# Performance work log

Hardware: AMD Instinct MI355X
Metric: run time of the kernel (lower is better)

## Reference

```python
import jax, jax.numpy as jnp
import numpy as np

# pywt db2 decomposition filters (mode='symmetric', pywt defaults)
DEC_LO = np.array([-0.12940952255092145, 0.22414386804185735,
                   0.836516303737469, 0.48296291314469025], dtype=np.float32)
DEC_HI = np.array([-0.48296291314469025, 0.836516303737469,
                   -0.22414386804185735, -0.12940952255092145], dtype=np.float32)


def _dwt_axis(x, filt, axis):
    """Single-level 1D DWT along `axis`, symmetric padding, matching pywt.

    Equivalent to: symmetric-pad by F-1 each side, full convolution with
    `filt` (true convolution => filter flipped), take indices 1,3,5,...
    Implemented as pad (F-2, F-1) + strided correlation with reversed filter.
    """
    F = filt.shape[0]
    x = jnp.moveaxis(x, axis, -1)
    N = x.shape[-1]
    out_len = (N + F - 1) // 2
    pad = [(0, 0)] * (x.ndim - 1) + [(F - 2, F - 1)]
    xp = jnp.pad(x, pad, mode='symmetric')
    filt_rev = filt[::-1]
    # sum of 4 strided slices (F=4) -- fully vectorized, no big intermediates
    out = filt_rev[0] * xp[..., 0:2 * out_len:2]
    for k in range(1, F):
        out = out + filt_rev[k] * xp[..., k:k + 2 * out_len:2]
    return jnp.moveaxis(out, -1, axis)


def setup_inputs() -> dict:
    key = jax.random.key(0)
    x = jax.random.normal(key, (16, 3, 1024, 1024), dtype=jnp.float32)
    return {"x": x}


def reference(x):
    lo = jnp.asarray(DEC_LO)
    hi = jnp.asarray(DEC_HI)
    # pywt.dwt2 -> cA = 'aa' (approx rows, approx cols),
    #              cH = 'da' (detail along axis -2, approx along axis -1)
    lo_rows = _dwt_axis(x, lo, -2)
    hi_rows = _dwt_axis(x, hi, -2)
    cA = _dwt_axis(lo_rows, lo, -1)
    cH = _dwt_axis(hi_rows, lo, -1)
    return (cA, cH)
```

## Files before the change

### kernel.cpp

```cpp
#include <hip/hip_runtime.h>


#define N 1024
#define NOUT 513
#define TI 8
#define STRIPS ((NOUT + TI - 1) / TI)

__device__ __forceinline__ int refl(int p) {
    int r = p - 2;
    r = (r < 0) ? (-1 - r) : r;
    r = (r > N - 1) ? (2 * N - 1 - r) : r;
    return r;
}

__device__ __forceinline__ float4 comb4(float w0, const float4 a, float w1, const float4 b,
                                        float w2, const float4 c, float w3, const float4 d) {
    float4 r;
    r.x = fmaf(w0, a.x, fmaf(w1, b.x, fmaf(w2, c.x, w3 * d.x)));
    r.y = fmaf(w0, a.y, fmaf(w1, b.y, fmaf(w2, c.y, w3 * d.y)));
    r.z = fmaf(w0, a.z, fmaf(w1, b.z, fmaf(w2, c.z, w3 * d.z)));
    r.w = fmaf(w0, a.w, fmaf(w1, b.w, fmaf(w2, c.w, w3 * d.w)));
    return r;
}

__device__ __forceinline__ float2 comb2(float w0, const float2 a, float w1, const float2 b,
                                        float w2, const float2 c, float w3, const float2 d) {
    float2 r;
    r.x = fmaf(w0, a.x, fmaf(w1, b.x, fmaf(w2, c.x, w3 * d.x)));
    r.y = fmaf(w0, a.y, fmaf(w1, b.y, fmaf(w2, c.y, w3 * d.y)));
    return r;
}

__global__ __launch_bounds__(128, 4) void dwt2_nolds(const float* __restrict__ x,
                                                     float* __restrict__ out) {
    const float l0 =  0.48296291314469025f;
    const float l1 =  0.836516303737469f;
    const float l2 =  0.22414386804185735f;
    const float l3 = -0.12940952255092145f;
    const float h0 = -0.12940952255092145f;
    const float h1 = -0.22414386804185735f;
    const float h2 =  0.836516303737469f;
    const float h3 = -0.48296291314469025f;

    const int strip = blockIdx.x;
    const int img   = blockIdx.y;
    const int i0 = strip * TI;
    const int u  = threadIdx.x;
    const int c  = 8 * u;
    const int ce = (u == 0) ? 0 : (c - 2);

    const float* xim = x + (size_t)img * N * N;
    const size_t plane = (size_t)NOUT * NOUT;
    float* cA = out + (size_t)img * plane;
    float* cH = out + ((size_t)48 + img) * plane;

    const int nrows = (NOUT - i0 < TI) ? (NOUT - i0) : TI;

    const float* p0 = xim + (size_t)refl(2 * i0)     * N;
    const float* p1 = xim + (size_t)refl(2 * i0 + 1) * N;
    const float* p2 = xim + (size_t)refl(2 * i0 + 2) * N;
    const float* p3 = xim + (size_t)refl(2 * i0 + 3) * N;

    float4 r0a = *reinterpret_cast<const float4*>(p0 + c);
    float4 r0b = *reinterpret_cast<const float4*>(p0 + c + 4);
    float2 r0e = *reinterpret_cast<const float2*>(p0 + ce);
    float4 r1a = *reinterpret_cast<const float4*>(p1 + c);
    float4 r1b = *reinterpret_cast<const float4*>(p1 + c + 4);
    float2 r1e = *reinterpret_cast<const float2*>(p1 + ce);
    float4 n0a = *reinterpret_cast<const float4*>(p2 + c);
    float4 n0b = *reinterpret_cast<const float4*>(p2 + c + 4);
    float2 n0e = *reinterpret_cast<const float2*>(p2 + ce);
    float4 n1a = *reinterpret_cast<const float4*>(p3 + c);
    float4 n1b = *reinterpret_cast<const float4*>(p3 + c + 4);
    float2 n1e = *reinterpret_cast<const float2*>(p3 + ce);

    for (int ii = 0; ii < nrows; ++ii) {
        const int i = i0 + ii;

        float4 vloA = comb4(l0, r0a, l1, r1a, l2, n0a, l3, n1a);
        float4 vloB = comb4(l0, r0b, l1, r1b, l2, n0b, l3, n1b);
        float2 plo  = comb2(l0, r0e, l1, r1e, l2, n0e, l3, n1e);
        float4 vhiA = comb4(h0, r0a, h1, r1a, h2, n0a, h3, n1a);
        float4 vhiB = comb4(h0, r0b, h1, r1b, h2, n0b, h3, n1b);
        float2 phi  = comb2(h0, r0e, h1, r1e, h2, n0e, h3, n1e);

        if (u == 0) {
            plo = make_float2(vloA.y, vloA.x);
            phi = make_float2(vhiA.y, vhiA.x);
        }

        r0a = n0a; r0b = n0b; r0e = n0e;
        r1a = n1a; r1b = n1b; r1e = n1e;
        if (ii + 1 < nrows) {
            const float* q0 = xim + (size_t)refl(2 * i + 4) * N;
            const float* q1 = xim + (size_t)refl(2 * i + 5) * N;
            n0a = *reinterpret_cast<const float4*>(q0 + c);
            n0b = *reinterpret_cast<const float4*>(q0 + c + 4);
            n0e = *reinterpret_cast<const float2*>(q0 + ce);
            n1a = *reinterpret_cast<const float4*>(q1 + c);
            n1b = *reinterpret_cast<const float4*>(q1 + c + 4);
            n1e = *reinterpret_cast<const float2*>(q1 + ce);
        }

        float oA0 = fmaf(l0, plo.x,  fmaf(l1, plo.y,  fmaf(l2, vloA.x, l3 * vloA.y)));
        float oA1 = fmaf(l0, vloA.x, fmaf(l1, vloA.y, fmaf(l2, vloA.z, l3 * vloA.w)));
        float oA2 = fmaf(l0, vloA.z, fmaf(l1, vloA.w, fmaf(l2, vloB.x, l3 * vloB.y)));
        float oA3 = fmaf(l0, vloB.x, fmaf(l1, vloB.y, fmaf(l2, vloB.z, l3 * vloB.w)));
        float oH0 = fmaf(l0, phi.x,  fmaf(l1, phi.y,  fmaf(l2, vhiA.x, l3 * vhiA.y)));
        float oH1 = fmaf(l0, vhiA.x, fmaf(l1, vhiA.y, fmaf(l2, vhiA.z, l3 * vhiA.w)));
        float oH2 = fmaf(l0, vhiA.z, fmaf(l1, vhiA.w, fmaf(l2, vhiB.x, l3 * vhiB.y)));
        float oH3 = fmaf(l0, vhiB.x, fmaf(l1, vhiB.y, fmaf(l2, vhiB.z, l3 * vhiB.w)));

        float* pa = cA + (size_t)i * NOUT + 4 * u;
        float* ph = cH + (size_t)i * NOUT + 4 * u;
        pa[0] = oA0; pa[1] = oA1; pa[2] = oA2; pa[3] = oA3;
        ph[0] = oH0; ph[1] = oH1; ph[2] = oH2; ph[3] = oH3;

        if (u == 127) {
            pa[4] = fmaf(l0, vloB.z, fmaf(l1, vloB.w, fmaf(l2, vloB.w, l3 * vloB.z)));
            ph[4] = fmaf(l0, vhiB.z, fmaf(l1, vhiB.w, fmaf(l2, vhiB.w, l3 * vhiB.z)));
        }
    }
}

extern "C" void kernel_launch(void* const* d_in, const int* in_sizes, int n_in,
                              void* d_out, int out_size, void* d_ws, size_t ws_size,
                              hipStream_t stream) {
    (void)in_sizes; (void)n_in; (void)d_ws; (void)ws_size; (void)out_size;
    const float* x = (const float*)d_in[0];
    float* out = (float*)d_out;
    dim3 grid(STRIPS, 48);
    dim3 block(128);
    dwt2_nolds<<<grid, block, 0, stream>>>(x, out);
}
```

Baseline: 316.0 us.

## Deepen row prefetch, double strip height, remap blocks across XCDs, nontemporal stores

Each block now processes 16 output rows instead of 8 and prefetches two row-pairs ahead rather than one, which lengthens the load pipeline and reduces redundant halo row reads between strips. The 2D grid is flattened into a 1D grid and remapped so consecutive block IDs are spread across eight groups, aiming for better locality per XCD. Output stores become nontemporal to avoid polluting cache with write-once data. The deeper prefetch raises register pressure, and the fewer, longer blocks may reduce parallelism and latency hiding.

```diff
diff --git a/kernel.cpp b/kernel.cpp
--- a/kernel.cpp
+++ b/kernel.cpp
@@ -3,8 +3,10 @@
 
 #define N 1024
 #define NOUT 513
-#define TI 8
+#define TI 16
 #define STRIPS ((NOUT + TI - 1) / TI)
+#define NIMG 48
+#define NBLK (STRIPS * NIMG)
 
 __device__ __forceinline__ int refl(int p) {
     int r = p - 2;
@@ -31,8 +33,8 @@
     return r;
 }
 
-__global__ __launch_bounds__(128, 4) void dwt2_nolds(const float* __restrict__ x,
-                                                     float* __restrict__ out) {
+__global__ __launch_bounds__(128, 4) void dwt2_deep(const float* __restrict__ x,
+                                                    float* __restrict__ out) {
     const float l0 =  0.48296291314469025f;
     const float l1 =  0.836516303737469f;
     const float l2 =  0.22414386804185735f;
@@ -42,8 +44,11 @@
     const float h2 =  0.836516303737469f;
     const float h3 = -0.48296291314469025f;
 
-    const int strip = blockIdx.x;
-    const int img   = blockIdx.y;
+    const int bid = blockIdx.x;
+    const int wg  = (bid & 7) * (NBLK / 8) + (bid >> 3);
+    const int img   = wg / STRIPS;
+    const int strip = wg % STRIPS;
+
     const int i0 = strip * TI;
     const int u  = threadIdx.x;
     const int c  = 8 * u;
@@ -52,7 +57,7 @@
     const float* xim = x + (size_t)img * N * N;
     const size_t plane = (size_t)NOUT * NOUT;
     float* cA = out + (size_t)img * plane;
-    float* cH = out + ((size_t)48 + img) * plane;
+    float* cH = out + ((size_t)NIMG + img) * plane;
 
     const int nrows = (NOUT - i0 < TI) ? (NOUT - i0) : TI;
 
@@ -60,46 +65,56 @@
     const float* p1 = xim + (size_t)refl(2 * i0 + 1) * N;
     const float* p2 = xim + (size_t)refl(2 * i0 + 2) * N;
     const float* p3 = xim + (size_t)refl(2 * i0 + 3) * N;
+    const float* p4 = xim + (size_t)refl(2 * i0 + 4) * N;
+    const float* p5 = xim + (size_t)refl(2 * i0 + 5) * N;
 
-    float4 r0a = *reinterpret_cast<const float4*>(p0 + c);
-    float4 r0b = *reinterpret_cast<const float4*>(p0 + c + 4);
-    float2 r0e = *reinterpret_cast<const float2*>(p0 + ce);
-    float4 r1a = *reinterpret_cast<const float4*>(p1 + c);
-    float4 r1b = *reinterpret_cast<const float4*>(p1 + c + 4);
-    float2 r1e = *reinterpret_cast<const float2*>(p1 + ce);
-    float4 n0a = *reinterpret_cast<const float4*>(p2 + c);
-    float4 n0b = *reinterpret_cast<const float4*>(p2 + c + 4);
-    float2 n0e = *reinterpret_cast<const float2*>(p2 + ce);
-    float4 n1a = *reinterpret_cast<const float4*>(p3 + c);
-    float4 n1b = *reinterpret_cast<const float4*>(p3 + c + 4);
-    float2 n1e = *reinterpret_cast<const float2*>(p3 + ce);
+    float4 a0a = *reinterpret_cast<const float4*>(p0 + c);
+    float4 a0b = *reinterpret_cast<const float4*>(p0 + c + 4);
+    float2 a0e = *reinterpret_cast<const float2*>(p0 + ce);
+    float4 a1a = *reinterpret_cast<const float4*>(p1 + c);
+    float4 a1b = *reinterpret_cast<const float4*>(p1 + c + 4);
+    float2 a1e = *reinterpret_cast<const float2*>(p1 + ce);
+    float4 b0a = *reinterpret_cast<const float4*>(p2 + c);
+    float4 b0b = *reinterpret_cast<const float4*>(p2 + c + 4);
+    float2 b0e = *reinterpret_cast<const float2*>(p2 + ce);
+    float4 b1a = *reinterpret_cast<const float4*>(p3 + c);
+    float4 b1b = *reinterpret_cast<const float4*>(p3 + c + 4);
+    float2 b1e = *reinterpret_cast<const float2*>(p3 + ce);
+    float4 c0a = *reinterpret_cast<const float4*>(p4 + c);
+    float4 c0b = *reinterpret_cast<const float4*>(p4 + c + 4);
+    float2 c0e = *reinterpret_cast<const float2*>(p4 + ce);
+    float4 c1a = *reinterpret_cast<const float4*>(p5 + c);
+    float4 c1b = *reinterpret_cast<const float4*>(p5 + c + 4);
+    float2 c1e = *reinterpret_cast<const float2*>(p5 + ce);
 
     for (int ii = 0; ii < nrows; ++ii) {
         const int i = i0 + ii;
 
-        float4 vloA = comb4(l0, r0a, l1, r1a, l2, n0a, l3, n1a);
-        float4 vloB = comb4(l0, r0b, l1, r1b, l2, n0b, l3, n1b);
-        float2 plo  = comb2(l0, r0e, l1, r1e, l2, n0e, l3, n1e);
-        float4 vhiA = comb4(h0, r0a, h1, r1a, h2, n0a, h3, n1a);
-        float4 vhiB = comb4(h0, r0b, h1, r1b, h2, n0b, h3, n1b);
-        float2 phi  = comb2(h0, r0e, h1, r1e, h2, n0e, h3, n1e);
+        float4 vloA = comb4(l0, a0a, l1, a1a, l2, b0a, l3, b1a);
+        float4 vloB = comb4(l0, a0b, l1, a1b, l2, b0b, l3, b1b);
+        float2 plo  = comb2(l0, a0e, l1, a1e, l2, b0e, l3, b1e);
+        float4 vhiA = comb4(h0, a0a, h1, a1a, h2, b0a, h3, b1a);
+        float4 vhiB = comb4(h0, a0b, h1, a1b, h2, b0b, h3, b1b);
+        float2 phi  = comb2(h0, a0e, h1, a1e, h2, b0e, h3, b1e);
 
         if (u == 0) {
             plo = make_float2(vloA.y, vloA.x);
             phi = make_float2(vhiA.y, vhiA.x);
         }
 
-        r0a = n0a; r0b = n0b; r0e = n0e;
-        r1a = n1a; r1b = n1b; r1e = n1e;
-        if (ii + 1 < nrows) {
-            const float* q0 = xim + (size_t)refl(2 * i + 4) * N;
-            const float* q1 = xim + (size_t)refl(2 * i + 5) * N;
-            n0a = *reinterpret_cast<const float4*>(q0 + c);
-            n0b = *reinterpret_cast<const float4*>(q0 + c + 4);
-            n0e = *reinterpret_cast<const float2*>(q0 + ce);
-            n1a = *reinterpret_cast<const float4*>(q1 + c);
-            n1b = *reinterpret_cast<const float4*>(q1 + c + 4);
-            n1e = *reinterpret_cast<const float2*>(q1 + ce);
+        a0a = b0a; a0b = b0b; a0e = b0e;
+        a1a = b1a; a1b = b1b; a1e = b1e;
+        b0a = c0a; b0b = c0b; b0e = c0e;
+        b1a = c1a; b1b = c1b; b1e = c1e;
+        if (ii + 2 < nrows) {
+            const float* q0 = xim + (size_t)refl(2 * i + 6) * N;
+            const float* q1 = xim + (size_t)refl(2 * i + 7) * N;
+            c0a = *reinterpret_cast<const float4*>(q0 + c);
+            c0b = *reinterpret_cast<const float4*>(q0 + c + 4);
+            c0e = *reinterpret_cast<const float2*>(q0 + ce);
+            c1a = *reinterpret_cast<const float4*>(q1 + c);
+            c1b = *reinterpret_cast<const float4*>(q1 + c + 4);
+            c1e = *reinterpret_cast<const float2*>(q1 + ce);
         }
 
         float oA0 = fmaf(l0, plo.x,  fmaf(l1, plo.y,  fmaf(l2, vloA.x, l3 * vloA.y)));
@@ -113,12 +128,20 @@
 
         float* pa = cA + (size_t)i * NOUT + 4 * u;
         float* ph = cH + (size_t)i * NOUT + 4 * u;
-        pa[0] = oA0; pa[1] = oA1; pa[2] = oA2; pa[3] = oA3;
-        ph[0] = oH0; ph[1] = oH1; ph[2] = oH2; ph[3] = oH3;
+        __builtin_nontemporal_store(oA0, pa + 0);
+        __builtin_nontemporal_store(oA1, pa + 1);
+        __builtin_nontemporal_store(oA2, pa + 2);
+        __builtin_nontemporal_store(oA3, pa + 3);
+        __builtin_nontemporal_store(oH0, ph + 0);
+        __builtin_nontemporal_store(oH1, ph + 1);
+        __builtin_nontemporal_store(oH2, ph + 2);
+        __builtin_nontemporal_store(oH3, ph + 3);
 
         if (u == 127) {
-            pa[4] = fmaf(l0, vloB.z, fmaf(l1, vloB.w, fmaf(l2, vloB.w, l3 * vloB.z)));
-            ph[4] = fmaf(l0, vhiB.z, fmaf(l1, vhiB.w, fmaf(l2, vhiB.w, l3 * vhiB.z)));
+            float eA = fmaf(l0, vloB.z, fmaf(l1, vloB.w, fmaf(l2, vloB.w, l3 * vloB.z)));
+            float eH = fmaf(l0, vhiB.z, fmaf(l1, vhiB.w, fmaf(l2, vhiB.w, l3 * vhiB.z)));
+            __builtin_nontemporal_store(eA, pa + 4);
+            __builtin_nontemporal_store(eH, ph + 4);
         }
     }
 }
@@ -129,7 +152,7 @@
     (void)in_sizes; (void)n_in; (void)d_ws; (void)ws_size; (void)out_size;
     const float* x = (const float*)d_in[0];
     float* out = (float*)d_out;
-    dim3 grid(STRIPS, 48);
+    dim3 grid(NBLK);
     dim3 block(128);
-    dwt2_nolds<<<grid, block, 0, stream>>>(x, out);
+    dwt2_deep<<<grid, block, 0, stream>>>(x, out);
 }
```

After: 325.4 us. +3.0%, slower.

## Halve per-thread columns and transpose outputs through LDS for coalesced stores

Applied to the files above, without the earlier changes.

Each thread now handles 4 input columns instead of 8, which doubles the block size to 256 threads and roughly halves per-thread register state. Output pairs are staged through a per-wave shared-memory buffer so each wave writes contiguous 64-float runs instead of strided 4-float scalar stores. The goal is better store coalescing and more occupancy. In exchange it adds LDS traffic, and relies on the wave's lockstep execution without a barrier between the LDS write and read.

```diff
diff --git a/kernel.cpp b/kernel.cpp
--- a/kernel.cpp
+++ b/kernel.cpp
@@ -5,6 +5,7 @@
 #define NOUT 513
 #define TI 8
 #define STRIPS ((NOUT + TI - 1) / TI)
+#define NIMG 48
 
 __device__ __forceinline__ int refl(int p) {
     int r = p - 2;
@@ -31,8 +32,8 @@
     return r;
 }
 
-__global__ __launch_bounds__(128, 4) void dwt2_nolds(const float* __restrict__ x,
-                                                     float* __restrict__ out) {
+__global__ __launch_bounds__(256, 8) void dwt2_v3(const float* __restrict__ x,
+                                                  float* __restrict__ out) {
     const float l0 =  0.48296291314469025f;
     const float l1 =  0.836516303737469f;
     const float l2 =  0.22414386804185735f;
@@ -42,17 +43,22 @@
     const float h2 =  0.836516303737469f;
     const float h3 = -0.48296291314469025f;
 
+    __shared__ float sA[4][128];
+    __shared__ float sH[4][128];
+
     const int strip = blockIdx.x;
     const int img   = blockIdx.y;
     const int i0 = strip * TI;
-    const int u  = threadIdx.x;
-    const int c  = 8 * u;
-    const int ce = (u == 0) ? 0 : (c - 2);
+    const int u    = threadIdx.x;
+    const int wave = u >> 6;
+    const int lane = u & 63;
+    const int c4 = 4 * u;
+    const int ce = (u == 0) ? 0 : (c4 - 2);
 
     const float* xim = x + (size_t)img * N * N;
     const size_t plane = (size_t)NOUT * NOUT;
     float* cA = out + (size_t)img * plane;
-    float* cH = out + ((size_t)48 + img) * plane;
+    float* cH = out + ((size_t)NIMG + img) * plane;
 
     const int nrows = (NOUT - i0 < TI) ? (NOUT - i0) : TI;
 
@@ -61,64 +67,64 @@
     const float* p2 = xim + (size_t)refl(2 * i0 + 2) * N;
     const float* p3 = xim + (size_t)refl(2 * i0 + 3) * N;
 
-    float4 r0a = *reinterpret_cast<const float4*>(p0 + c);
-    float4 r0b = *reinterpret_cast<const float4*>(p0 + c + 4);
-    float2 r0e = *reinterpret_cast<const float2*>(p0 + ce);
-    float4 r1a = *reinterpret_cast<const float4*>(p1 + c);
-    float4 r1b = *reinterpret_cast<const float4*>(p1 + c + 4);
-    float2 r1e = *reinterpret_cast<const float2*>(p1 + ce);
-    float4 n0a = *reinterpret_cast<const float4*>(p2 + c);
-    float4 n0b = *reinterpret_cast<const float4*>(p2 + c + 4);
-    float2 n0e = *reinterpret_cast<const float2*>(p2 + ce);
-    float4 n1a = *reinterpret_cast<const float4*>(p3 + c);
-    float4 n1b = *reinterpret_cast<const float4*>(p3 + c + 4);
-    float2 n1e = *reinterpret_cast<const float2*>(p3 + ce);
+    float4 a0m = *reinterpret_cast<const float4*>(p0 + c4);
+    float2 a0e = *reinterpret_cast<const float2*>(p0 + ce);
+    float4 a1m = *reinterpret_cast<const float4*>(p1 + c4);
+    float2 a1e = *reinterpret_cast<const float2*>(p1 + ce);
+    float4 b0m = *reinterpret_cast<const float4*>(p2 + c4);
+    float2 b0e = *reinterpret_cast<const float2*>(p2 + ce);
+    float4 b1m = *reinterpret_cast<const float4*>(p3 + c4);
+    float2 b1e = *reinterpret_cast<const float2*>(p3 + ce);
 
     for (int ii = 0; ii < nrows; ++ii) {
         const int i = i0 + ii;
 
-        float4 vloA = comb4(l0, r0a, l1, r1a, l2, n0a, l3, n1a);
-        float4 vloB = comb4(l0, r0b, l1, r1b, l2, n0b, l3, n1b);
-        float2 plo  = comb2(l0, r0e, l1, r1e, l2, n0e, l3, n1e);
-        float4 vhiA = comb4(h0, r0a, h1, r1a, h2, n0a, h3, n1a);
-        float4 vhiB = comb4(h0, r0b, h1, r1b, h2, n0b, h3, n1b);
-        float2 phi  = comb2(h0, r0e, h1, r1e, h2, n0e, h3, n1e);
+        float4 vloM = comb4(l0, a0m, l1, a1m, l2, b0m, l3, b1m);
+        float2 vloE = comb2(l0, a0e, l1, a1e, l2, b0e, l3, b1e);
+        float4 vhiM = comb4(h0, a0m, h1, a1m, h2, b0m, h3, b1m);
+        float2 vhiE = comb2(h0, a0e, h1, a1e, h2, b0e, h3, b1e);
 
         if (u == 0) {
-            plo = make_float2(vloA.y, vloA.x);
-            phi = make_float2(vhiA.y, vhiA.x);
+            vloE = make_float2(vloM.y, vloM.x);
+            vhiE = make_float2(vhiM.y, vhiM.x);
         }
 
-        r0a = n0a; r0b = n0b; r0e = n0e;
-        r1a = n1a; r1b = n1b; r1e = n1e;
+        a0m = b0m; a0e = b0e;
+        a1m = b1m; a1e = b1e;
         if (ii + 1 < nrows) {
             const float* q0 = xim + (size_t)refl(2 * i + 4) * N;
             const float* q1 = xim + (size_t)refl(2 * i + 5) * N;
-            n0a = *reinterpret_cast<const float4*>(q0 + c);
-            n0b = *reinterpret_cast<const float4*>(q0 + c + 4);
-            n0e = *reinterpret_cast<const float2*>(q0 + ce);
-            n1a = *reinterpret_cast<const float4*>(q1 + c);
-            n1b = *reinterpret_cast<const float4*>(q1 + c + 4);
-            n1e = *reinterpret_cast<const float2*>(q1 + ce);
+            b0m = *reinterpret_cast<const float4*>(q0 + c4);
+            b0e = *reinterpret_cast<const float2*>(q0 + ce);
+            b1m = *reinterpret_cast<const float4*>(q1 + c4);
+            b1e = *reinterpret_cast<const float2*>(q1 + ce);
         }
 
-        float oA0 = fmaf(l0, plo.x,  fmaf(l1, plo.y,  fmaf(l2, vloA.x, l3 * vloA.y)));
-        float oA1 = fmaf(l0, vloA.x, fmaf(l1, vloA.y, fmaf(l2, vloA.z, l3 * vloA.w)));
-        float oA2 = fmaf(l0, vloA.z, fmaf(l1, vloA.w, fmaf(l2, vloB.x, l3 * vloB.y)));
-        float oA3 = fmaf(l0, vloB.x, fmaf(l1, vloB.y, fmaf(l2, vloB.z, l3 * vloB.w)));
-        float oH0 = fmaf(l0, phi.x,  fmaf(l1, phi.y,  fmaf(l2, vhiA.x, l3 * vhiA.y)));
-        float oH1 = fmaf(l0, vhiA.x, fmaf(l1, vhiA.y, fmaf(l2, vhiA.z, l3 * vhiA.w)));
-        float oH2 = fmaf(l0, vhiA.z, fmaf(l1, vhiA.w, fmaf(l2, vhiB.x, l3 * vhiB.y)));
-        float oH3 = fmaf(l0, vhiB.x, fmaf(l1, vhiB.y, fmaf(l2, vhiB.z, l3 * vhiB.w)));
+        float oA0 = fmaf(l0, vloE.x, fmaf(l1, vloE.y, fmaf(l2, vloM.x, l3 * vloM.y)));
+        float oA1 = fmaf(l0, vloM.x, fmaf(l1, vloM.y, fmaf(l2, vloM.z, l3 * vloM.w)));
+        float oH0 = fmaf(l0, vhiE.x, fmaf(l1, vhiE.y, fmaf(l2, vhiM.x, l3 * vhiM.y)));
+        float oH1 = fmaf(l0, vhiM.x, fmaf(l1, vhiM.y, fmaf(l2, vhiM.z, l3 * vhiM.w)));
 
-        float* pa = cA + (size_t)i * NOUT + 4 * u;
-        float* ph = cH + (size_t)i * NOUT + 4 * u;
-        pa[0] = oA0; pa[1] = oA1; pa[2] = oA2; pa[3] = oA3;
-        ph[0] = oH0; ph[1] = oH1; ph[2] = oH2; ph[3] = oH3;
+        sA[wave][2 * lane]     = oA0;
+        sA[wave][2 * lane + 1] = oA1;
+        sH[wave][2 * lane]     = oH0;
+        sH[wave][2 * lane + 1] = oH1;
+        float rA0 = sA[wave][lane];
+        float rA1 = sA[wave][64 + lane];
+        float rH0 = sH[wave][lane];
+        float rH1 = sH[wave][64 + lane];
 
-        if (u == 127) {
-            pa[4] = fmaf(l0, vloB.z, fmaf(l1, vloB.w, fmaf(l2, vloB.w, l3 * vloB.z)));
-            ph[4] = fmaf(l0, vhiB.z, fmaf(l1, vhiB.w, fmaf(l2, vhiB.w, l3 * vhiB.z)));
+        const int j0 = (wave << 7) + lane;
+        float* pa = cA + (size_t)i * NOUT;
+        float* ph = cH + (size_t)i * NOUT;
+        pa[j0]      = rA0;
+        pa[j0 + 64] = rA1;
+        ph[j0]      = rH0;
+        ph[j0 + 64] = rH1;
+
+        if (u == 255) {
+            pa[512] = fmaf(l0, vloM.z, fmaf(l1, vloM.w, fmaf(l2, vloM.w, l3 * vloM.z)));
+            ph[512] = fmaf(l0, vhiM.z, fmaf(l1, vhiM.w, fmaf(l2, vhiM.w, l3 * vhiM.z)));
         }
     }
 }
@@ -129,7 +135,7 @@
     (void)in_sizes; (void)n_in; (void)d_ws; (void)ws_size; (void)out_size;
     const float* x = (const float*)d_in[0];
     float* out = (float*)d_out;
-    dim3 grid(STRIPS, 48);
-    dim3 block(128);
-    dwt2_nolds<<<grid, block, 0, stream>>>(x, out);
+    dim3 grid(STRIPS, NIMG);
+    dim3 block(256);
+    dwt2_v3<<<grid, block, 0, stream>>>(x, out);
 }
```

Measured after the change: 310.7 us. Within noise of the previous version (-1.7%).
